# Kernel tuning notes

Measured on AMD Instinct MI355X. Metric: run time of the kernel, lower is better.

The kernel has to match this reference:

```python
import jax, jax.numpy as jnp
import numpy as np

B, T, D, DH, DFF = 4, 2048, 1024, 1024, 4096


def setup_inputs() -> dict:
    key = jax.random.key(0)
    ks = jax.random.split(key, 8)
    s = 0.02
    return {
        "x": jax.random.normal(ks[0], (B, T, D), jnp.float32),
        "ln1_g": jnp.ones((D,), jnp.float32),
        "ln1_b": jnp.zeros((D,), jnp.float32),
        "W_q": jax.random.normal(ks[1], (D, DH), jnp.float32) * s,
        "b_q": jnp.zeros((DH,), jnp.float32),
        "W_k": jax.random.normal(ks[2], (D, DH), jnp.float32) * s,
        "b_k": jnp.zeros((DH,), jnp.float32),
        "W_v": jax.random.normal(ks[3], (D, DH), jnp.float32) * s,
        "b_v": jnp.zeros((DH,), jnp.float32),
        "ln2_g": jnp.ones((D,), jnp.float32),
        "ln2_b": jnp.zeros((D,), jnp.float32),
        "W_in": jax.random.normal(ks[4], (D, DFF), jnp.float32) * s,
        "b_in": jnp.zeros((DFF,), jnp.float32),
        "W_out": jax.random.normal(ks[5], (DFF, D), jnp.float32) * s,
        "b_out": jnp.zeros((D,), jnp.float32),
    }


def _layernorm(x, g, b, eps=1e-5):
    mu = jnp.mean(x, axis=-1, keepdims=True)
    var = jnp.var(x, axis=-1, keepdims=True)
    return (x - mu) * jax.lax.rsqrt(var + eps) * g + b


def reference(x, ln1_g, ln1_b, W_q, b_q, W_k, b_k, W_v, b_v,
              ln2_g, ln2_b, W_in, b_in, W_out, b_out):
    # --- attention branch (pre-LN) ---
    h = _layernorm(x, ln1_g, ln1_b)                      # [B,T,D]
    Q = h @ W_q + b_q                                    # [B,T,DH]
    K = h @ W_k + b_k
    V = h @ W_v + b_v
    scale = 1.0 / jnp.sqrt(jnp.asarray(K.shape[-1], h.dtype))
    att = jnp.einsum("btd,bsd->bts", Q, K) * scale       # [B,T,T]
    # NOTE: source calls att.masked_fill(...) without assignment -> mask
    # is discarded; faithfully no causal mask applied here.
    att = jax.nn.softmax(att, axis=-1)
    attn_out = jnp.einsum("bts,bsd->btd", att, V)        # [B,T,DH]
    x = x + attn_out
    # --- MLP branch (pre-LN) ---
    h2 = _layernorm(x, ln2_g, ln2_b)
    ff = jax.nn.gelu(h2 @ W_in + b_in, approximate=False)
    x = x + (ff @ W_out + b_out)
    return x
```

## Files before the change

kernel.cpp:

```cpp
#include <hip/hip_runtime.h>
#include <hip/hip_bf16.h>

#define B_    4
#define T_    2048
#define D_    1024
#define DH_   1024
#define DFF_  4096
#define MTOT  (B_ * T_)

using f32x4  = __attribute__((ext_vector_type(4))) float;
using bf16x8 = __attribute__((ext_vector_type(8))) short;

__device__ __forceinline__ unsigned short f2bf(float f) {
    unsigned u = __builtin_bit_cast(unsigned, f);
    u += 0x7fffu + ((u >> 16) & 1u);
    return (unsigned short)(u >> 16);
}
__device__ __forceinline__ float bf2f(unsigned short h) {
    unsigned u = ((unsigned)h) << 16;
    return __builtin_bit_cast(float, u);
}

__device__ __forceinline__ void gload16(const short* g, short* l) {
    __builtin_amdgcn_global_load_lds(
        (const __attribute__((address_space(1))) unsigned int*)g,
        (__attribute__((address_space(3))) unsigned int*)l, 16, 0, 0);
}

__global__ __launch_bounds__(256) void transp_f32_bf16(
    const float* __restrict__ src, short* __restrict__ dst, int K, int N) {
    __shared__ float tile[32][33];
    int tk = blockIdx.y * 32, tn = blockIdx.x * 32;
    int tx = threadIdx.x & 31, ty = threadIdx.x >> 5;
#pragma unroll
    for (int i = 0; i < 4; i++) {
        int r = ty + i * 8;
        tile[r][tx] = src[(size_t)(tk + r) * N + tn + tx];
    }
    __syncthreads();
#pragma unroll
    for (int i = 0; i < 4; i++) {
        int r = ty + i * 8;
        dst[(size_t)(tn + r) * K + tk + tx] = f2bf(tile[tx][r]);
    }
}

__global__ void copyv(const float* __restrict__ s, float* __restrict__ d, int n) {
    int i = blockIdx.x * blockDim.x + threadIdx.x;
    if (i < n) d[i] = s[i];
}

__global__ __launch_bounds__(256) void ln_rows(
    const float* __restrict__ x, const float* __restrict__ g,
    const float* __restrict__ bta, short* __restrict__ out) {
    int row = blockIdx.x;
    const float* xr = x + (size_t)row * D_;
    int t = threadIdx.x;
    float4 v = *(const float4*)(xr + t * 4);
    float s  = v.x + v.y + v.z + v.w;
    float s2 = v.x * v.x + v.y * v.y + v.z * v.z + v.w * v.w;
#pragma unroll
    for (int off = 1; off < 64; off <<= 1) {
        s  += __shfl_xor(s, off);
        s2 += __shfl_xor(s2, off);
    }
    __shared__ float as_[4], as2_[4];
    int wave = t >> 6, lane = t & 63;
    if (lane == 0) { as_[wave] = s; as2_[wave] = s2; }
    __syncthreads();
    s  = as_[0] + as_[1] + as_[2] + as_[3];
    s2 = as2_[0] + as2_[1] + as2_[2] + as2_[3];
    float mean = s * (1.0f / D_);
    float var  = s2 * (1.0f / D_) - mean * mean;
    float rstd = rsqrtf(var + 1e-5f);
    float4 gv = *(const float4*)(g + t * 4);
    float4 bv = *(const float4*)(bta + t * 4);
    short4 o;
    o.x = f2bf((v.x - mean) * rstd * gv.x + bv.x);
    o.y = f2bf((v.y - mean) * rstd * gv.y + bv.y);
    o.z = f2bf((v.z - mean) * rstd * gv.z + bv.z);
    o.w = f2bf((v.w - mean) * rstd * gv.w + bv.w);
    *(short4*)(out + (size_t)row * D_ + t * 4) = o;
}

template<int NB, int BIAS_MODE, int ACT, int RES, int OUT_BF16>
__global__ __launch_bounds__(512, 2) void gemmT(
    const short* __restrict__ A, int lda, long long sA,
    const short* __restrict__ Bt, int ldb, long long sB,
    void* __restrict__ C, int ldc, long long sC,
    const float* __restrict__ bias,
    const float* __restrict__ res, int ldr, long long sR,
    int K) {
    extern __shared__ short smem_[];
    short* shA = smem_;
    short* shB = smem_ + (NB == 4 ? 32768 : 49152);
    const int SB = 4096 * NB;

    int gx = gridDim.x, gy = gridDim.y;
    int n2d = gx * gy;
    int nwg = n2d * gridDim.z;
    int lid = blockIdx.x + gx * (blockIdx.y + gy * blockIdx.z);
    int q = nwg >> 3, rq = nwg & 7, xcd = lid & 7, i_ = lid >> 3;
    int nid = (xcd < rq ? xcd * (q + 1) : rq * (q + 1) + (xcd - rq) * q) + i_;
    int z = nid / n2d, r2d = nid % n2d;
    int sw = gy << 2;
    int strip = r2d / sw, rr = r2d % sw;
    int by = rr >> 2, bx = (strip << 2) + (rr & 3);

    int bm = by * 256, bn = bx * (64 * NB);
    const short* gA = A  + (size_t)z * sA + (size_t)bm * lda;
    const short* gB = Bt + (size_t)z * sB + (size_t)bn * ldb;
    int tid = threadIdx.x, lane = tid & 63, w = tid >> 6;
    int wr = w >> 2, wc = w & 3;

    int rbase = tid >> 3;
    int gcol  = ((((tid & 7) << 4) ^ ((rbase & 7) << 4)) >> 1);
    const short* pA[4]; const short* pB[4];
#pragma unroll
    for (int c = 0; c < 4; c++)
        pA[c] = gA + (size_t)(c * 64 + rbase) * lda + gcol;
#pragma unroll
    for (int c = 0; c < NB; c++)
        pB[c] = gB + (size_t)(c * 64 + rbase) * ldb + gcol;

    int aoff[8], boff[4];
#pragma unroll
    for (int f = 0; f < 8; f++) {
        int row = wr * 128 + f * 16 + (lane & 15);
        aoff[f] = row * 128 + ((((lane >> 4) * 16)) ^ ((row & 7) << 4));
    }
#pragma unroll
    for (int f = 0; f < NB; f++) {
        int row = wc * (16 * NB) + f * 16 + (lane & 15);
        boff[f] = row * 128 + ((((lane >> 4) * 16)) ^ ((row & 7) << 4));
    }

    int nk = K >> 6;
    f32x4 acc[8][NB] = {};

#define MFROW(r_, av) \
    _Pragma("unroll") \
    for (int n_ = 0; n_ < NB; n_++) \
        acc[r_][n_] = __builtin_amdgcn_mfma_f32_16x16x32_bf16(av, bfv[n_], acc[r_][n_], 0, 0, 0);

    if constexpr (NB == 4) {
#pragma unroll
        for (int c = 0; c < 4; c++) gload16(pA[c], shA + c * 4096 + tid * 8);
#pragma unroll
        for (int c = 0; c < 4; c++) gload16(pB[c], shB + c * 4096 + tid * 8);
        asm volatile("s_waitcnt vmcnt(0)" ::: "memory");
        __builtin_amdgcn_s_barrier();

        for (int t = 0; t < nk; t++) {
            const char* sA_ = (const char*)(shA + (t & 1) * 16384);
            const char* sB_ = (const char*)(shB + (t & 1) * SB);
            short* wA = shA + ((t + 1) & 1) * 16384;
            short* wB = shB + ((t + 1) & 1) * SB;
            int ks = (t + 1 < nk ? t + 1 : nk - 1) << 6;
            bf16x8 af[4], bfv[4];

#pragma unroll
            for (int f = 0; f < 4; f++) af[f] = *(const bf16x8*)(sA_ + aoff[f]);
#pragma unroll
            for (int f = 0; f < 4; f++) bfv[f] = *(const bf16x8*)(sB_ + boff[f]);
            gload16(pA[0] + ks, wA + tid * 8);
            gload16(pA[2] + ks, wA + 2 * 4096 + tid * 8);
            __builtin_amdgcn_s_barrier();
            asm volatile("s_waitcnt lgkmcnt(0)" ::: "memory");
            __builtin_amdgcn_s_setprio(1);
            MFROW(0, af[0]) MFROW(1, af[1]) MFROW(2, af[2]) MFROW(3, af[3])
            __builtin_amdgcn_s_setprio(0);
            asm volatile("s_waitcnt vmcnt(2)" ::: "memory");
            __builtin_amdgcn_s_barrier();
#pragma unroll
            for (int f = 0; f < 4; f++) af[f] = *(const bf16x8*)(sA_ + aoff[4 + f]);
            gload16(pB[0] + ks, wB + tid * 8);
            gload16(pB[1] + ks, wB + 4096 + tid * 8);
            __builtin_amdgcn_s_barrier();
            asm volatile("s_waitcnt lgkmcnt(0)" ::: "memory");
            __builtin_amdgcn_s_setprio(1);
            MFROW(4, af[0]) MFROW(5, af[1]) MFROW(6, af[2]) MFROW(7, af[3])
            __builtin_amdgcn_s_setprio(0);
            __builtin_amdgcn_s_barrier();
#pragma unroll
            for (int f = 0; f < 4; f++) af[f] = *(const bf16x8*)(sA_ + (aoff[f] ^ 64));
#pragma unroll
            for (int f = 0; f < 4; f++) bfv[f] = *(const bf16x8*)(sB_ + (boff[f] ^ 64));
            gload16(pB[2] + ks, wB + 2 * 4096 + tid * 8);
            gload16(pB[3] + ks, wB + 3 * 4096 + tid * 8);
            __builtin_amdgcn_s_barrier();
            asm volatile("s_waitcnt lgkmcnt(0)" ::: "memory");
            __builtin_amdgcn_s_setprio(1);
            MFROW(0, af[0]) MFROW(1, af[1]) MFROW(2, af[2]) MFROW(3, af[3])
            __builtin_amdgcn_s_setprio(0);
            __builtin_amdgcn_s_barrier();
#pragma unroll
            for (int f = 0; f < 4; f++) af[f] = *(const bf16x8*)(sA_ + (aoff[4 + f] ^ 64));
            gload16(pA[1] + ks, wA + 4096 + tid * 8);
            gload16(pA[3] + ks, wA + 3 * 4096 + tid * 8);
            __builtin_amdgcn_s_barrier();
            asm volatile("s_waitcnt lgkmcnt(0)" ::: "memory");
            __builtin_amdgcn_s_setprio(1);
            MFROW(4, af[0]) MFROW(5, af[1]) MFROW(6, af[2]) MFROW(7, af[3])
            __builtin_amdgcn_s_setprio(0);
            asm volatile("s_waitcnt vmcnt(2)" ::: "memory");
            __builtin_amdgcn_s_barrier();
        }
    } else {
#pragma unroll
        for (int s = 0; s < 2; s++) {
#pragma unroll
            for (int c = 0; c < 4; c++)
                gload16(pA[c] + s * 64, shA + s * 16384 + c * 4096 + tid * 8);
#pragma unroll
            for (int c = 0; c < 2; c++)
                gload16(pB[c] + s * 64, shB + s * 8192 + c * 4096 + tid * 8);
        }
        asm volatile("s_waitcnt vmcnt(6)" ::: "memory");
        __builtin_amdgcn_s_barrier();

        for (int t = 0; t < nk; t++) {
            int rs = t % 3, es = (t + 2) % 3;
            const char* sA_ = (const char*)(shA + rs * 16384);
            const char* sB_ = (const char*)(shB + rs * 8192);
            short* wA = shA + es * 16384;
            short* wB = shB + es * 8192;
            int ks = (t + 2 < nk ? t + 2 : nk - 1) << 6;
            bf16x8 af[8], bfv[2];

#pragma unroll
            for (int f = 0; f < 8; f++) af[f] = *(const bf16x8*)(sA_ + aoff[f]);
#pragma unroll
            for (int f = 0; f < 2; f++) bfv[f] = *(const bf16x8*)(sB_ + boff[f]);
            gload16(pA[0] + ks, wA + tid * 8);
            gload16(pA[1] + ks, wA + 4096 + tid * 8);
            gload16(pA[2] + ks, wA + 2 * 4096 + tid * 8);
            gload16(pA[3] + ks, wA + 3 * 4096 + tid * 8);
            gload16(pB[0] + ks, wB + tid * 8);
            gload16(pB[1] + ks, wB + 4096 + tid * 8);
            __builtin_amdgcn_s_barrier();
            asm volatile("s_waitcnt lgkmcnt(0)" ::: "memory");
            __builtin_amdgcn_s_setprio(1);
            MFROW(0, af[0]) MFROW(1, af[1]) MFROW(2, af[2]) MFROW(3, af[3])
            MFROW(4, af[4]) MFROW(5, af[5]) MFROW(6, af[6]) MFROW(7, af[7])
            __builtin_amdgcn_s_setprio(0);
            __builtin_amdgcn_s_barrier();
#pragma unroll
            for (int f = 0; f < 8; f++) af[f] = *(const bf16x8*)(sA_ + (aoff[f] ^ 64));
#pragma unroll
            for (int f = 0; f < 2; f++) bfv[f] = *(const bf16x8*)(sB_ + (boff[f] ^ 64));
            __builtin_amdgcn_s_barrier();
            asm volatile("s_waitcnt lgkmcnt(0)" ::: "memory");
            __builtin_amdgcn_s_setprio(1);
            MFROW(0, af[0]) MFROW(1, af[1]) MFROW(2, af[2]) MFROW(3, af[3])
            MFROW(4, af[4]) MFROW(5, af[5]) MFROW(6, af[6]) MFROW(7, af[7])
            __builtin_amdgcn_s_setprio(0);
            asm volatile("s_waitcnt vmcnt(6)" ::: "memory");
            __builtin_amdgcn_s_barrier();
        }
    }
#undef MFROW
    asm volatile("s_waitcnt vmcnt(0)" ::: "memory");

    size_t zc = (size_t)z * (size_t)sC;
    float* lpart = (float*)smem_;
#pragma unroll
    for (int fr = 0; fr < 8; fr++) {
        float pr[4] = {0.f, 0.f, 0.f, 0.f};
        float s8[4];
        if (RES == 2) {
#pragma unroll
            for (int r_ = 0; r_ < 4; r_++) {
                int row = bm + wr * 128 + fr * 16 + (lane >> 4) * 4 + r_;
                float s = 0.f;
#pragma unroll
                for (int i = 0; i < 8; i++) s += bias[((size_t)z * 8 + i) * 2048 + row];
                s8[r_] = 1.0f / s;
            }
        }
#pragma unroll
        for (int fn = 0; fn < NB; fn++) {
            int colc = bn + wc * (16 * NB) + fn * 16 + (lane & 15);
#pragma unroll
            for (int r_ = 0; r_ < 4; r_++) {
                int row = bm + wr * 128 + fr * 16 + (lane >> 4) * 4 + r_;
                float v = acc[fr][fn][r_];
                if (BIAS_MODE == 1) v += bias[colc];
                else if (BIAS_MODE == 2) v += bias[row];
                if (ACT == 1) v = 0.5f * v * (1.0f + erff(v * 0.70710678118654752f));
                if (ACT == 2) {
                    v = expf(v * 0.03125f);
                    unsigned short us = f2bf(v);
                    ((short*)C)[zc + (size_t)row * ldc + colc] = (short)us;
                    pr[r_] += bf2f(us);
                    continue;
                }
                if (RES == 1) v += res[(size_t)z * sR + (size_t)row * ldr + colc];
                if (RES == 2) v = v * s8[r_] + res[(size_t)z * sR + (size_t)row * ldr + colc];
                if (OUT_BF16) ((short*)C)[zc + (size_t)row * ldc + colc] = f2bf(v);
                else          ((float*)C)[zc + (size_t)row * ldc + colc] = v;
            }
        }
        if (ACT == 2) {
#pragma unroll
            for (int m_ = 1; m_ < 16; m_ <<= 1) {
#pragma unroll
                for (int r_ = 0; r_ < 4; r_++) pr[r_] += __shfl_xor(pr[r_], m_);
            }
            if ((lane & 15) == 0) {
#pragma unroll
                for (int r_ = 0; r_ < 4; r_++)
                    lpart[wc * 256 + wr * 128 + fr * 16 + (lane >> 4) * 4 + r_] = pr[r_];
            }
        }
    }
    if (ACT == 2) {
        __syncthreads();
        if (tid < 256) {
            float s = lpart[tid] + lpart[256 + tid] + lpart[512 + tid] + lpart[768 + tid];
            ((float*)res)[((size_t)z * 8 + bx) * 2048 + bm + tid] = s;
        }
    }
}

#define SHB4 131072
#define SHB2 147456

extern "C" void kernel_launch(void* const* d_in, const int* in_sizes, int n_in,
                              void* d_out, int out_size, void* d_ws, size_t ws_size,
                              hipStream_t stream) {
    const float* x    = (const float*)d_in[0];
    const float* ln1g = (const float*)d_in[1];
    const float* ln1b = (const float*)d_in[2];
    const float* Wq   = (const float*)d_in[3];
    const float* bq   = (const float*)d_in[4];
    const float* Wk   = (const float*)d_in[5];
    const float* bk   = (const float*)d_in[6];
    const float* Wv   = (const float*)d_in[7];
    const float* bv   = (const float*)d_in[8];
    const float* ln2g = (const float*)d_in[9];
    const float* ln2b = (const float*)d_in[10];
    const float* Win  = (const float*)d_in[11];
    const float* bin  = (const float*)d_in[12];
    const float* Wout = (const float*)d_in[13];
    const float* bout = (const float*)d_in[14];

    char* ws = (char*)d_ws;
    size_t off = 0;
    auto alloc = [&](size_t bytes) {
        void* p = ws + off;
        off += (bytes + 255) & ~(size_t)255;
        return p;
    };
    short* WqkT  = (short*)alloc((size_t)2048 * 1024 * 2);
    short* WvT   = (short*)alloc((size_t)1024 * 1024 * 2);
    short* WinT  = (short*)alloc((size_t)4096 * 1024 * 2);
    short* WoutT = (short*)alloc((size_t)1024 * 4096 * 2);
    float* bqk   = (float*)alloc((size_t)2048 * 4);
    short* h     = (short*)alloc((size_t)MTOT * 1024 * 2);
    short* QK    = (short*)alloc((size_t)MTOT * 2048 * 2);
    short* VT    = (short*)alloc((size_t)1024 * 8192 * 2);
    float* S     = (float*)alloc((size_t)4 * 2048 * 2048 * 4);
    float* x1    = (float*)alloc((size_t)MTOT * 1024 * 4);
    float* rowsums = (float*)alloc((size_t)4 * 8 * 2048 * 4);
    (void)ws_size; (void)in_sizes; (void)n_in; (void)out_size;

    hipFuncSetAttribute((const void*)gemmT<4,1,0,0,1>, hipFuncAttributeMaxDynamicSharedMemorySize, SHB4);
    hipFuncSetAttribute((const void*)gemmT<4,0,2,0,1>, hipFuncAttributeMaxDynamicSharedMemorySize, SHB4);
    hipFuncSetAttribute((const void*)gemmT<4,1,1,0,1>, hipFuncAttributeMaxDynamicSharedMemorySize, SHB4);
    hipFuncSetAttribute((const void*)gemmT<2,2,0,0,1>, hipFuncAttributeMaxDynamicSharedMemorySize, SHB2);
    hipFuncSetAttribute((const void*)gemmT<2,0,0,2,0>, hipFuncAttributeMaxDynamicSharedMemorySize, SHB2);
    hipFuncSetAttribute((const void*)gemmT<2,1,0,1,0>, hipFuncAttributeMaxDynamicSharedMemorySize, SHB2);

    transp_f32_bf16<<<dim3(32, 32), 256, 0, stream>>>(Wq, WqkT, 1024, 1024);
    transp_f32_bf16<<<dim3(32, 32), 256, 0, stream>>>(Wk, WqkT + (size_t)1024 * 1024, 1024, 1024);
    transp_f32_bf16<<<dim3(32, 32), 256, 0, stream>>>(Wv, WvT, 1024, 1024);
    transp_f32_bf16<<<dim3(128, 32), 256, 0, stream>>>(Win, WinT, 1024, 4096);
    transp_f32_bf16<<<dim3(32, 128), 256, 0, stream>>>(Wout, WoutT, 4096, 1024);
    copyv<<<4, 256, 0, stream>>>(bq, bqk, 1024);
    copyv<<<4, 256, 0, stream>>>(bk, bqk + 1024, 1024);

    ln_rows<<<MTOT, 256, 0, stream>>>(x, ln1g, ln1b, h);

    gemmT<4, 1, 0, 0, 1><<<dim3(8, 32, 1), 512, SHB4, stream>>>(
        h, 1024, 0, WqkT, 1024, 0, QK, 2048, 0, bqk, nullptr, 0, 0, 1024);

    gemmT<2, 2, 0, 0, 1><<<dim3(64, 4, 1), 512, SHB2, stream>>>(
        WvT, 1024, 0, h, 1024, 0, VT, 8192, 0, bv, nullptr, 0, 0, 1024);

    gemmT<4, 0, 2, 0, 1><<<dim3(8, 8, 4), 512, SHB4, stream>>>(
        QK, 2048, 4194304LL, QK + 1024, 2048, 4194304LL,
        (short*)S, 4096, 8388608LL, nullptr, (const float*)rowsums, 0, 0, 1024);

    gemmT<2, 0, 0, 2, 0><<<dim3(8, 8, 4), 512, SHB2, stream>>>(
        (short*)S, 4096, 8388608LL, VT, 8192, 2048LL,
        x1, 1024, 2097152LL, rowsums, x, 1024, 2097152LL, 2048);

    ln_rows<<<MTOT, 256, 0, stream>>>(x1, ln2g, ln2b, h);

    short* ff = (short*)S;
    gemmT<4, 1, 1, 0, 1><<<dim3(16, 32, 1), 512, SHB4, stream>>>(
        h, 1024, 0, WinT, 1024, 0, ff, 4096, 0, bin, nullptr, 0, 0, 1024);

    gemmT<2, 1, 0, 1, 0><<<dim3(8, 32, 1), 512, SHB2, stream>>>(
        ff, 4096, 0, WoutT, 4096, 0, (float*)d_out, 1024, 0, bout,
        x1, 1024, 0, 4096);
}
```

Measured before the change: 393.1 us.

## Deepen NB=4 GEMM prefetch pipeline to triple-buffered A with staggered B loads

The NB=4 GEMM path moves from a double-buffered single-stage prefetch to a deeper pipeline. A tiles are triple-buffered and fetched two k-steps ahead. B halves are split so half of the next tile and half of the tile after that are in flight, and the wait relaxes to vmcnt(6). This hides more global-load latency behind MFMA work. It raises LDS use from 128KB to 160KB per block, which may limit occupancy, given launch_bounds asks for 2 blocks per CU.

```diff
diff --git a/kernel.cpp b/kernel.cpp
--- a/kernel.cpp
+++ b/kernel.cpp
@@ -93,7 +93,7 @@
     int K) {
     extern __shared__ short smem_[];
     short* shA = smem_;
-    short* shB = smem_ + (NB == 4 ? 32768 : 49152);
+    short* shB = smem_ + 49152;
     const int SB = 4096 * NB;
 
     int gx = gridDim.x, gy = gridDim.y;
@@ -144,38 +144,49 @@
         acc[r_][n_] = __builtin_amdgcn_mfma_f32_16x16x32_bf16(av, bfv[n_], acc[r_][n_], 0, 0, 0);
 
     if constexpr (NB == 4) {
-#pragma unroll
-        for (int c = 0; c < 4; c++) gload16(pA[c], shA + c * 4096 + tid * 8);
-#pragma unroll
-        for (int c = 0; c < 4; c++) gload16(pB[c], shB + c * 4096 + tid * 8);
-        asm volatile("s_waitcnt vmcnt(0)" ::: "memory");
+        gload16(pA[0], shA + 0 * 4096 + tid * 8);
+        gload16(pA[2], shA + 2 * 4096 + tid * 8);
+        gload16(pA[1], shA + 1 * 4096 + tid * 8);
+        gload16(pA[3], shA + 3 * 4096 + tid * 8);
+        gload16(pB[0], shB + 0 * 4096 + tid * 8);
+        gload16(pB[1], shB + 1 * 4096 + tid * 8);
+        gload16(pB[2], shB + 2 * 4096 + tid * 8);
+        gload16(pB[3], shB + 3 * 4096 + tid * 8);
+        gload16(pA[0] + 64, shA + 16384 + 0 * 4096 + tid * 8);
+        gload16(pA[2] + 64, shA + 16384 + 2 * 4096 + tid * 8);
+        gload16(pA[1] + 64, shA + 16384 + 1 * 4096 + tid * 8);
+        gload16(pA[3] + 64, shA + 16384 + 3 * 4096 + tid * 8);
+        gload16(pB[0] + 64, shB + 16384 + 0 * 4096 + tid * 8);
+        gload16(pB[1] + 64, shB + 16384 + 1 * 4096 + tid * 8);
+        asm volatile("s_waitcnt vmcnt(6)" ::: "memory");
         __builtin_amdgcn_s_barrier();
 
         for (int t = 0; t < nk; t++) {
-            const char* sA_ = (const char*)(shA + (t & 1) * 16384);
-            const char* sB_ = (const char*)(shB + (t & 1) * SB);
-            short* wA = shA + ((t + 1) & 1) * 16384;
-            short* wB = shB + ((t + 1) & 1) * SB;
-            int ks = (t + 1 < nk ? t + 1 : nk - 1) << 6;
+            const char* sA_ = (const char*)(shA + (t % 3) * 16384);
+            const char* sB_ = (const char*)(shB + (t & 1) * 16384);
+            short* wA2 = shA + ((t + 2) % 3) * 16384;
+            short* wB1 = shB + ((t + 1) & 1) * 16384;
+            short* wB2 = shB + (t & 1) * 16384;
+            int ka  = (t + 2 < nk ? t + 2 : nk - 1) << 6;
+            int kb1 = (t + 1 < nk ? t + 1 : nk - 1) << 6;
             bf16x8 af[4], bfv[4];
 
 #pragma unroll
             for (int f = 0; f < 4; f++) af[f] = *(const bf16x8*)(sA_ + aoff[f]);
 #pragma unroll
             for (int f = 0; f < 4; f++) bfv[f] = *(const bf16x8*)(sB_ + boff[f]);
-            gload16(pA[0] + ks, wA + tid * 8);
-            gload16(pA[2] + ks, wA + 2 * 4096 + tid * 8);
+            gload16(pB[2] + kb1, wB1 + 2 * 4096 + tid * 8);
+            gload16(pB[3] + kb1, wB1 + 3 * 4096 + tid * 8);
             __builtin_amdgcn_s_barrier();
             asm volatile("s_waitcnt lgkmcnt(0)" ::: "memory");
             __builtin_amdgcn_s_setprio(1);
             MFROW(0, af[0]) MFROW(1, af[1]) MFROW(2, af[2]) MFROW(3, af[3])
             __builtin_amdgcn_s_setprio(0);
-            asm volatile("s_waitcnt vmcnt(2)" ::: "memory");
             __builtin_amdgcn_s_barrier();
 #pragma unroll
             for (int f = 0; f < 4; f++) af[f] = *(const bf16x8*)(sA_ + aoff[4 + f]);
-            gload16(pB[0] + ks, wB + tid * 8);
-            gload16(pB[1] + ks, wB + 4096 + tid * 8);
+            gload16(pA[0] + ka, wA2 + 0 * 4096 + tid * 8);
+            gload16(pA[2] + ka, wA2 + 2 * 4096 + tid * 8);
             __builtin_amdgcn_s_barrier();
             asm volatile("s_waitcnt lgkmcnt(0)" ::: "memory");
             __builtin_amdgcn_s_setprio(1);
@@ -186,8 +197,8 @@
             for (int f = 0; f < 4; f++) af[f] = *(const bf16x8*)(sA_ + (aoff[f] ^ 64));
 #pragma unroll
             for (int f = 0; f < 4; f++) bfv[f] = *(const bf16x8*)(sB_ + (boff[f] ^ 64));
-            gload16(pB[2] + ks, wB + 2 * 4096 + tid * 8);
-            gload16(pB[3] + ks, wB + 3 * 4096 + tid * 8);
+            gload16(pA[1] + ka, wA2 + 1 * 4096 + tid * 8);
+            gload16(pA[3] + ka, wA2 + 3 * 4096 + tid * 8);
             __builtin_amdgcn_s_barrier();
             asm volatile("s_waitcnt lgkmcnt(0)" ::: "memory");
             __builtin_amdgcn_s_setprio(1);
@@ -196,14 +207,14 @@
             __builtin_amdgcn_s_barrier();
 #pragma unroll
             for (int f = 0; f < 4; f++) af[f] = *(const bf16x8*)(sA_ + (aoff[4 + f] ^ 64));
-            gload16(pA[1] + ks, wA + 4096 + tid * 8);
-            gload16(pA[3] + ks, wA + 3 * 4096 + tid * 8);
+            gload16(pB[0] + ka, wB2 + 0 * 4096 + tid * 8);
+            gload16(pB[1] + ka, wB2 + 1 * 4096 + tid * 8);
             __builtin_amdgcn_s_barrier();
             asm volatile("s_waitcnt lgkmcnt(0)" ::: "memory");
             __builtin_amdgcn_s_setprio(1);
             MFROW(4, af[0]) MFROW(5, af[1]) MFROW(6, af[2]) MFROW(7, af[3])
             __builtin_amdgcn_s_setprio(0);
-            asm volatile("s_waitcnt vmcnt(2)" ::: "memory");
+            asm volatile("s_waitcnt vmcnt(6)" ::: "memory");
             __builtin_amdgcn_s_barrier();
         }
     } else {
@@ -323,7 +334,7 @@
     }
 }
 
-#define SHB4 131072
+#define SHB4 163840
 #define SHB2 147456
 
 extern "C" void kernel_launch(void* const* d_in, const int* in_sizes, int n_in,
```

Measured after the change: 391.3 us. No clear change (-0.5%).

## Unify GEMM into 256x128 tile, 256-thread kernel with triple-buffered K=32 pipeline

Applied to the files above, without the earlier changes.

Replaces the two GEMM variants (256x256 and 256x128 tiles, 512 threads) with a single 256-thread kernel that computes 256x128 tiles. It uses a three-stage LDS ring with K-step 32 and register double-buffering of the B fragments, which cuts shared memory per block so more blocks can reside per CU. Grids are resized to match, and the softmax row-sum partials grow from 8 to 16 per row. Each wave now carries a 128x64 accumulator, which raises register pressure. The smaller K step and smaller tiles also mean more barriers and less data reuse per block.

```diff
diff --git a/kernel.cpp b/kernel.cpp
--- a/kernel.cpp
+++ b/kernel.cpp
@@ -83,8 +83,8 @@
     *(short4*)(out + (size_t)row * D_ + t * 4) = o;
 }
 
-template<int NB, int BIAS_MODE, int ACT, int RES, int OUT_BF16>
-__global__ __launch_bounds__(512, 2) void gemmT(
+template<int BIAS_MODE, int ACT, int RES, int OUT_BF16>
+__global__ __launch_bounds__(256, 2) void gemmT(
     const short* __restrict__ A, int lda, long long sA,
     const short* __restrict__ Bt, int ldb, long long sB,
     void* __restrict__ C, int ldc, long long sC,
@@ -93,8 +93,7 @@
     int K) {
     extern __shared__ short smem_[];
     short* shA = smem_;
-    short* shB = smem_ + (NB == 4 ? 32768 : 49152);
-    const int SB = 4096 * NB;
+    short* shB = smem_ + 24576;
 
     int gx = gridDim.x, gy = gridDim.y;
     int n2d = gx * gy;
@@ -107,160 +106,116 @@
     int strip = r2d / sw, rr = r2d % sw;
     int by = rr >> 2, bx = (strip << 2) + (rr & 3);
 
-    int bm = by * 256, bn = bx * (64 * NB);
+    int bm = by * 256, bn = bx * 128;
     const short* gA = A  + (size_t)z * sA + (size_t)bm * lda;
     const short* gB = Bt + (size_t)z * sB + (size_t)bn * ldb;
     int tid = threadIdx.x, lane = tid & 63, w = tid >> 6;
-    int wr = w >> 2, wc = w & 3;
-
-    int rbase = tid >> 3;
-    int gcol  = ((((tid & 7) << 4) ^ ((rbase & 7) << 4)) >> 1);
-    const short* pA[4]; const short* pB[4];
+    int wr = w >> 1, wc = w & 1;
+
+    int rbase = tid >> 2;
+    int gcol  = ((((tid & 3) << 4) ^ (((rbase >> 1) & 3) << 4)) >> 1);
+    const short* pA[4]; const short* pB[2];
 #pragma unroll
     for (int c = 0; c < 4; c++)
         pA[c] = gA + (size_t)(c * 64 + rbase) * lda + gcol;
 #pragma unroll
-    for (int c = 0; c < NB; c++)
+    for (int c = 0; c < 2; c++)
         pB[c] = gB + (size_t)(c * 64 + rbase) * ldb + gcol;
 
     int aoff[8], boff[4];
 #pragma unroll
     for (int f = 0; f < 8; f++) {
         int row = wr * 128 + f * 16 + (lane & 15);
-        aoff[f] = row * 128 + ((((lane >> 4) * 16)) ^ ((row & 7) << 4));
-    }
-#pragma unroll
-    for (int f = 0; f < NB; f++) {
-        int row = wc * (16 * NB) + f * 16 + (lane & 15);
-        boff[f] = row * 128 + ((((lane >> 4) * 16)) ^ ((row & 7) << 4));
-    }
-
-    int nk = K >> 6;
-    f32x4 acc[8][NB] = {};
-
-#define MFROW(r_, av) \
-    _Pragma("unroll") \
-    for (int n_ = 0; n_ < NB; n_++) \
-        acc[r_][n_] = __builtin_amdgcn_mfma_f32_16x16x32_bf16(av, bfv[n_], acc[r_][n_], 0, 0, 0);
-
-    if constexpr (NB == 4) {
-#pragma unroll
-        for (int c = 0; c < 4; c++) gload16(pA[c], shA + c * 4096 + tid * 8);
-#pragma unroll
-        for (int c = 0; c < 4; c++) gload16(pB[c], shB + c * 4096 + tid * 8);
-        asm volatile("s_waitcnt vmcnt(0)" ::: "memory");
-        __builtin_amdgcn_s_barrier();
-
-        for (int t = 0; t < nk; t++) {
-            const char* sA_ = (const char*)(shA + (t & 1) * 16384);
-            const char* sB_ = (const char*)(shB + (t & 1) * SB);
-            short* wA = shA + ((t + 1) & 1) * 16384;
-            short* wB = shB + ((t + 1) & 1) * SB;
-            int ks = (t + 1 < nk ? t + 1 : nk - 1) << 6;
-            bf16x8 af[4], bfv[4];
-
-#pragma unroll
-            for (int f = 0; f < 4; f++) af[f] = *(const bf16x8*)(sA_ + aoff[f]);
-#pragma unroll
-            for (int f = 0; f < 4; f++) bfv[f] = *(const bf16x8*)(sB_ + boff[f]);
-            gload16(pA[0] + ks, wA + tid * 8);
-            gload16(pA[2] + ks, wA + 2 * 4096 + tid * 8);
-            __builtin_amdgcn_s_barrier();
-            asm volatile("s_waitcnt lgkmcnt(0)" ::: "memory");
-            __builtin_amdgcn_s_setprio(1);
-            MFROW(0, af[0]) MFROW(1, af[1]) MFROW(2, af[2]) MFROW(3, af[3])
-            __builtin_amdgcn_s_setprio(0);
-            asm volatile("s_waitcnt vmcnt(2)" ::: "memory");
-            __builtin_amdgcn_s_barrier();
-#pragma unroll
-            for (int f = 0; f < 4; f++) af[f] = *(const bf16x8*)(sA_ + aoff[4 + f]);
-            gload16(pB[0] + ks, wB + tid * 8);
-            gload16(pB[1] + ks, wB + 4096 + tid * 8);
-            __builtin_amdgcn_s_barrier();
-            asm volatile("s_waitcnt lgkmcnt(0)" ::: "memory");
-            __builtin_amdgcn_s_setprio(1);
-            MFROW(4, af[0]) MFROW(5, af[1]) MFROW(6, af[2]) MFROW(7, af[3])
-            __builtin_amdgcn_s_setprio(0);
-            __builtin_amdgcn_s_barrier();
-#pragma unroll
-            for (int f = 0; f < 4; f++) af[f] = *(const bf16x8*)(sA_ + (aoff[f] ^ 64));
-#pragma unroll
-            for (int f = 0; f < 4; f++) bfv[f] = *(const bf16x8*)(sB_ + (boff[f] ^ 64));
-            gload16(pB[2] + ks, wB + 2 * 4096 + tid * 8);
-            gload16(pB[3] + ks, wB + 3 * 4096 + tid * 8);
-            __builtin_amdgcn_s_barrier();
-            asm volatile("s_waitcnt lgkmcnt(0)" ::: "memory");
-            __builtin_amdgcn_s_setprio(1);
-            MFROW(0, af[0]) MFROW(1, af[1]) MFROW(2, af[2]) MFROW(3, af[3])
-            __builtin_amdgcn_s_setprio(0);
-            __builtin_amdgcn_s_barrier();
-#pragma unroll
-            for (int f = 0; f < 4; f++) af[f] = *(const bf16x8*)(sA_ + (aoff[4 + f] ^ 64));
-            gload16(pA[1] + ks, wA + 4096 + tid * 8);
-            gload16(pA[3] + ks, wA + 3 * 4096 + tid * 8);
-            __builtin_amdgcn_s_barrier();
-            asm volatile("s_waitcnt lgkmcnt(0)" ::: "memory");
-            __builtin_amdgcn_s_setprio(1);
-            MFROW(4, af[0]) MFROW(5, af[1]) MFROW(6, af[2]) MFROW(7, af[3])
-            __builtin_amdgcn_s_setprio(0);
-            asm volatile("s_waitcnt vmcnt(2)" ::: "memory");
-            __builtin_amdgcn_s_barrier();
-        }
-    } else {
-#pragma unroll
-        for (int s = 0; s < 2; s++) {
-#pragma unroll
-            for (int c = 0; c < 4; c++)
-                gload16(pA[c] + s * 64, shA + s * 16384 + c * 4096 + tid * 8);
-#pragma unroll
-            for (int c = 0; c < 2; c++)
-                gload16(pB[c] + s * 64, shB + s * 8192 + c * 4096 + tid * 8);
-        }
-        asm volatile("s_waitcnt vmcnt(6)" ::: "memory");
-        __builtin_amdgcn_s_barrier();
-
-        for (int t = 0; t < nk; t++) {
-            int rs = t % 3, es = (t + 2) % 3;
-            const char* sA_ = (const char*)(shA + rs * 16384);
-            const char* sB_ = (const char*)(shB + rs * 8192);
-            short* wA = shA + es * 16384;
-            short* wB = shB + es * 8192;
-            int ks = (t + 2 < nk ? t + 2 : nk - 1) << 6;
-            bf16x8 af[8], bfv[2];
-
-#pragma unroll
-            for (int f = 0; f < 8; f++) af[f] = *(const bf16x8*)(sA_ + aoff[f]);
-#pragma unroll
-            for (int f = 0; f < 2; f++) bfv[f] = *(const bf16x8*)(sB_ + boff[f]);
-            gload16(pA[0] + ks, wA + tid * 8);
-            gload16(pA[1] + ks, wA + 4096 + tid * 8);
-            gload16(pA[2] + ks, wA + 2 * 4096 + tid * 8);
-            gload16(pA[3] + ks, wA + 3 * 4096 + tid * 8);
-            gload16(pB[0] + ks, wB + tid * 8);
-            gload16(pB[1] + ks, wB + 4096 + tid * 8);
-            __builtin_amdgcn_s_barrier();
-            asm volatile("s_waitcnt lgkmcnt(0)" ::: "memory");
-            __builtin_amdgcn_s_setprio(1);
-            MFROW(0, af[0]) MFROW(1, af[1]) MFROW(2, af[2]) MFROW(3, af[3])
-            MFROW(4, af[4]) MFROW(5, af[5]) MFROW(6, af[6]) MFROW(7, af[7])
-            __builtin_amdgcn_s_setprio(0);
-            __builtin_amdgcn_s_barrier();
-#pragma unroll
-            for (int f = 0; f < 8; f++) af[f] = *(const bf16x8*)(sA_ + (aoff[f] ^ 64));
-#pragma unroll
-            for (int f = 0; f < 2; f++) bfv[f] = *(const bf16x8*)(sB_ + (boff[f] ^ 64));
-            __builtin_amdgcn_s_barrier();
-            asm volatile("s_waitcnt lgkmcnt(0)" ::: "memory");
-            __builtin_amdgcn_s_setprio(1);
-            MFROW(0, af[0]) MFROW(1, af[1]) MFROW(2, af[2]) MFROW(3, af[3])
-            MFROW(4, af[4]) MFROW(5, af[5]) MFROW(6, af[6]) MFROW(7, af[7])
-            __builtin_amdgcn_s_setprio(0);
-            asm volatile("s_waitcnt vmcnt(6)" ::: "memory");
-            __builtin_amdgcn_s_barrier();
-        }
-    }
-#undef MFROW
+        aoff[f] = row * 64 + (((lane >> 4) * 16) ^ (((row >> 1) & 3) << 4));
+    }
+#pragma unroll
+    for (int f = 0; f < 4; f++) {
+        int row = wc * 64 + f * 16 + (lane & 15);
+        boff[f] = row * 64 + (((lane >> 4) * 16) ^ (((row >> 1) & 3) << 4));
+    }
+
+    int nk = K >> 5;
+    f32x4 acc[8][4] = {};
+
+#pragma unroll
+    for (int s = 0; s < 2; s++) {
+#pragma unroll
+        for (int c = 0; c < 4; c++)
+            gload16(pA[c] + s * 32, shA + s * 8192 + c * 2048 + tid * 8);
+#pragma unroll
+        for (int c = 0; c < 2; c++)
+            gload16(pB[c] + s * 32, shB + s * 4096 + c * 2048 + tid * 8);
+    }
+    asm volatile("s_waitcnt vmcnt(6)" ::: "memory");
+    __builtin_amdgcn_s_barrier();
+
+    bf16x8 aA[4], aB[4], b0[4], b1[4];
+    {
+        const char* s0A = (const char*)shA;
+        const char* s0B = (const char*)shB;
+#pragma unroll
+        for (int f = 0; f < 4; f++) aA[f] = *(const bf16x8*)(s0A + aoff[f]);
+#pragma unroll
+        for (int f = 0; f < 4; f++) b0[f] = *(const bf16x8*)(s0B + boff[f]);
+        asm volatile("s_waitcnt lgkmcnt(0)" ::: "memory");
+    }
+
+#define MF(r_, av, bv) \
+    acc[r_][0] = __builtin_amdgcn_mfma_f32_16x16x32_bf16(av, bv[0], acc[r_][0], 0, 0, 0); \
+    acc[r_][1] = __builtin_amdgcn_mfma_f32_16x16x32_bf16(av, bv[1], acc[r_][1], 0, 0, 0); \
+    acc[r_][2] = __builtin_amdgcn_mfma_f32_16x16x32_bf16(av, bv[2], acc[r_][2], 0, 0, 0); \
+    acc[r_][3] = __builtin_amdgcn_mfma_f32_16x16x32_bf16(av, bv[3], acc[r_][3], 0, 0, 0);
+
+#define TILE(T, BUSE, BREAD) { \
+    int t = (T); \
+    const char* sA_  = (const char*)(shA + (t % 3) * 8192); \
+    const char* sA1_ = (const char*)(shA + ((t + 1) % 3) * 8192); \
+    const char* sB1_ = (const char*)(shB + ((t + 1) % 3) * 4096); \
+    short* wA2 = shA + ((t + 2) % 3) * 8192; \
+    short* wB2 = shB + ((t + 2) % 3) * 4096; \
+    int ks = (t + 2 < nk ? t + 2 : nk - 1) << 5; \
+     \
+    aB[0] = *(const bf16x8*)(sA_ + aoff[4]); \
+    aB[1] = *(const bf16x8*)(sA_ + aoff[5]); \
+    aB[2] = *(const bf16x8*)(sA_ + aoff[6]); \
+    aB[3] = *(const bf16x8*)(sA_ + aoff[7]); \
+    gload16(pA[0] + ks, wA2 + 0 * 2048 + tid * 8); \
+    gload16(pA[1] + ks, wA2 + 1 * 2048 + tid * 8); \
+    asm volatile("s_waitcnt lgkmcnt(4)" ::: "memory"); \
+    __builtin_amdgcn_sched_barrier(0); \
+    __builtin_amdgcn_s_setprio(1); \
+    MF(0, aA[0], BUSE) MF(1, aA[1], BUSE) MF(2, aA[2], BUSE) MF(3, aA[3], BUSE) \
+    __builtin_amdgcn_s_setprio(0); \
+    asm volatile("s_waitcnt vmcnt(2)" ::: "memory"); \
+    __builtin_amdgcn_s_barrier(); \
+     \
+    aA[0] = *(const bf16x8*)(sA1_ + aoff[0]); \
+    aA[1] = *(const bf16x8*)(sA1_ + aoff[1]); \
+    aA[2] = *(const bf16x8*)(sA1_ + aoff[2]); \
+    aA[3] = *(const bf16x8*)(sA1_ + aoff[3]); \
+    BREAD[0] = *(const bf16x8*)(sB1_ + boff[0]); \
+    BREAD[1] = *(const bf16x8*)(sB1_ + boff[1]); \
+    BREAD[2] = *(const bf16x8*)(sB1_ + boff[2]); \
+    BREAD[3] = *(const bf16x8*)(sB1_ + boff[3]); \
+    gload16(pA[2] + ks, wA2 + 2 * 2048 + tid * 8); \
+    gload16(pA[3] + ks, wA2 + 3 * 2048 + tid * 8); \
+    gload16(pB[0] + ks, wB2 + 0 * 2048 + tid * 8); \
+    gload16(pB[1] + ks, wB2 + 1 * 2048 + tid * 8); \
+    asm volatile("s_waitcnt lgkmcnt(8)" ::: "memory"); \
+    __builtin_amdgcn_sched_barrier(0); \
+    __builtin_amdgcn_s_setprio(1); \
+    MF(4, aB[0], BUSE) MF(5, aB[1], BUSE) MF(6, aB[2], BUSE) MF(7, aB[3], BUSE) \
+    __builtin_amdgcn_s_setprio(0); \
+    __builtin_amdgcn_s_barrier(); }
+
+    for (int tp = 0; tp < nk; tp += 2) {
+        TILE(tp,     b0, b1)
+        TILE(tp + 1, b1, b0)
+    }
+#undef TILE
+#undef MF
     asm volatile("s_waitcnt vmcnt(0)" ::: "memory");
+    __syncthreads();
 
     size_t zc = (size_t)z * (size_t)sC;
     float* lpart = (float*)smem_;
@@ -274,13 +229,13 @@
                 int row = bm + wr * 128 + fr * 16 + (lane >> 4) * 4 + r_;
                 float s = 0.f;
 #pragma unroll
-                for (int i = 0; i < 8; i++) s += bias[((size_t)z * 8 + i) * 2048 + row];
+                for (int i = 0; i < 16; i++) s += bias[((size_t)z * 16 + i) * 2048 + row];
                 s8[r_] = 1.0f / s;
             }
         }
 #pragma unroll
-        for (int fn = 0; fn < NB; fn++) {
-            int colc = bn + wc * (16 * NB) + fn * 16 + (lane & 15);
+        for (int fn = 0; fn < 4; fn++) {
+            int colc = bn + wc * 64 + fn * 16 + (lane & 15);
 #pragma unroll
             for (int r_ = 0; r_ < 4; r_++) {
                 int row = bm + wr * 128 + fr * 16 + (lane >> 4) * 4 + r_;
@@ -317,14 +272,13 @@
     if (ACT == 2) {
         __syncthreads();
         if (tid < 256) {
-            float s = lpart[tid] + lpart[256 + tid] + lpart[512 + tid] + lpart[768 + tid];
-            ((float*)res)[((size_t)z * 8 + bx) * 2048 + bm + tid] = s;
+            float s = lpart[tid] + lpart[256 + tid];
+            ((float*)res)[((size_t)z * 16 + bx) * 2048 + bm + tid] = s;
         }
     }
 }
 
-#define SHB4 131072
-#define SHB2 147456
+#define SHB 73728
 
 extern "C" void kernel_launch(void* const* d_in, const int* in_sizes, int n_in,
                               void* d_out, int out_size, void* d_ws, size_t ws_size,
@@ -362,15 +316,15 @@
     short* VT    = (short*)alloc((size_t)1024 * 8192 * 2);
     float* S     = (float*)alloc((size_t)4 * 2048 * 2048 * 4);
     float* x1    = (float*)alloc((size_t)MTOT * 1024 * 4);
-    float* rowsums = (float*)alloc((size_t)4 * 8 * 2048 * 4);
+    float* rowsums = (float*)alloc((size_t)4 * 16 * 2048 * 4);
     (void)ws_size; (void)in_sizes; (void)n_in; (void)out_size;
 
-    hipFuncSetAttribute((const void*)gemmT<4,1,0,0,1>, hipFuncAttributeMaxDynamicSharedMemorySize, SHB4);
-    hipFuncSetAttribute((const void*)gemmT<4,0,2,0,1>, hipFuncAttributeMaxDynamicSharedMemorySize, SHB4);
-    hipFuncSetAttribute((const void*)gemmT<4,1,1,0,1>, hipFuncAttributeMaxDynamicSharedMemorySize, SHB4);
-    hipFuncSetAttribute((const void*)gemmT<2,2,0,0,1>, hipFuncAttributeMaxDynamicSharedMemorySize, SHB2);
-    hipFuncSetAttribute((const void*)gemmT<2,0,0,2,0>, hipFuncAttributeMaxDynamicSharedMemorySize, SHB2);
-    hipFuncSetAttribute((const void*)gemmT<2,1,0,1,0>, hipFuncAttributeMaxDynamicSharedMemorySize, SHB2);
+    hipFuncSetAttribute((const void*)gemmT<1,0,0,1>, hipFuncAttributeMaxDynamicSharedMemorySize, SHB);
+    hipFuncSetAttribute((const void*)gemmT<2,0,0,1>, hipFuncAttributeMaxDynamicSharedMemorySize, SHB);
+    hipFuncSetAttribute((const void*)gemmT<0,2,0,1>, hipFuncAttributeMaxDynamicSharedMemorySize, SHB);
+    hipFuncSetAttribute((const void*)gemmT<0,0,2,0>, hipFuncAttributeMaxDynamicSharedMemorySize, SHB);
+    hipFuncSetAttribute((const void*)gemmT<1,1,0,1>, hipFuncAttributeMaxDynamicSharedMemorySize, SHB);
+    hipFuncSetAttribute((const void*)gemmT<1,0,1,0>, hipFuncAttributeMaxDynamicSharedMemorySize, SHB);
 
     transp_f32_bf16<<<dim3(32, 32), 256, 0, stream>>>(Wq, WqkT, 1024, 1024);
     transp_f32_bf16<<<dim3(32, 32), 256, 0, stream>>>(Wk, WqkT + (size_t)1024 * 1024, 1024, 1024);
@@ -382,27 +336,27 @@
 
     ln_rows<<<MTOT, 256, 0, stream>>>(x, ln1g, ln1b, h);
 
-    gemmT<4, 1, 0, 0, 1><<<dim3(8, 32, 1), 512, SHB4, stream>>>(
+    gemmT<1, 0, 0, 1><<<dim3(16, 32, 1), 256, SHB, stream>>>(
         h, 1024, 0, WqkT, 1024, 0, QK, 2048, 0, bqk, nullptr, 0, 0, 1024);
 
-    gemmT<2, 2, 0, 0, 1><<<dim3(64, 4, 1), 512, SHB2, stream>>>(
+    gemmT<2, 0, 0, 1><<<dim3(64, 4, 1), 256, SHB, stream>>>(
         WvT, 1024, 0, h, 1024, 0, VT, 8192, 0, bv, nullptr, 0, 0, 1024);
 
-    gemmT<4, 0, 2, 0, 1><<<dim3(8, 8, 4), 512, SHB4, stream>>>(
+    gemmT<0, 2, 0, 1><<<dim3(16, 8, 4), 256, SHB, stream>>>(
         QK, 2048, 4194304LL, QK + 1024, 2048, 4194304LL,
         (short*)S, 4096, 8388608LL, nullptr, (const float*)rowsums, 0, 0, 1024);
 
-    gemmT<2, 0, 0, 2, 0><<<dim3(8, 8, 4), 512, SHB2, stream>>>(
+    gemmT<0, 0, 2, 0><<<dim3(8, 8, 4), 256, SHB, stream>>>(
         (short*)S, 4096, 8388608LL, VT, 8192, 2048LL,
         x1, 1024, 2097152LL, rowsums, x, 1024, 2097152LL, 2048);
 
     ln_rows<<<MTOT, 256, 0, stream>>>(x1, ln2g, ln2b, h);
 
     short* ff = (short*)S;
-    gemmT<4, 1, 1, 0, 1><<<dim3(16, 32, 1), 512, SHB4, stream>>>(
+    gemmT<1, 1, 0, 1><<<dim3(32, 32, 1), 256, SHB, stream>>>(
         h, 1024, 0, WinT, 1024, 0, ff, 4096, 0, bin, nullptr, 0, 0, 1024);
 
-    gemmT<2, 1, 0, 1, 0><<<dim3(8, 32, 1), 512, SHB2, stream>>>(
+    gemmT<1, 0, 1, 0><<<dim3(8, 32, 1), 256, SHB, stream>>>(
         ff, 4096, 0, WoutT, 4096, 0, (float*)d_out, 1024, 0, bout,
         x1, 1024, 0, 4096);
 }
```

Measured after the change: 413.7 us. 1.05x slower.
